# Optimization experiments

Hardware: AMD Instinct MI355X
Metric: run time of the kernel (lower is better)

The kernel has to match this reference:

```python
import jax, jax.numpy as jnp
import numpy as np

C = 1024
H = 16

def setup_inputs() -> dict:
    key = jax.random.key(0)
    ks = jax.random.split(key, 12)
    s = lambda d: 1.0 / np.sqrt(d)
    return {
        "x": jax.random.normal(ks[0], (2, 2048, C), dtype=jnp.float32),
        "ln1_g": jnp.ones((C,), jnp.float32),
        "ln1_b": jnp.zeros((C,), jnp.float32),
        "attn_w": jax.random.normal(ks[1], (C, 3 * C), jnp.float32) * s(C),
        "attn_b": jnp.zeros((3 * C,), jnp.float32),
        "proj_w": jax.random.normal(ks[2], (C, C), jnp.float32) * s(C),
        "proj_b": jnp.zeros((C,), jnp.float32),
        "ln2_g": jnp.ones((C,), jnp.float32),
        "ln2_b": jnp.zeros((C,), jnp.float32),
        "fc_w": jax.random.normal(ks[3], (C, 4 * C), jnp.float32) * s(C),
        "fc_b": jnp.zeros((4 * C,), jnp.float32),
        "fc2_w": jax.random.normal(ks[4], (4 * C, C), jnp.float32) * s(4 * C),
        "fc2_b": jnp.zeros((C,), jnp.float32),
    }

def _layernorm(x, g, b, eps=1e-5):
    mu = jnp.mean(x, axis=-1, keepdims=True)
    var = jnp.var(x, axis=-1, keepdims=True)
    return (x - mu) * jax.lax.rsqrt(var + eps) * g + b

def _attn(x, attn_w, attn_b, proj_w, proj_b):
    B, T, Cd = x.shape
    hd = Cd // H
    qkv = x @ attn_w + attn_b                      # [B,T,3C]
    q, k, v = jnp.split(qkv, 3, axis=-1)
    q = q.reshape(B, T, H, hd).transpose(0, 2, 1, 3)  # [B,H,T,hd]
    k = k.reshape(B, T, H, hd).transpose(0, 2, 1, 3)
    v = v.reshape(B, T, H, hd).transpose(0, 2, 1, 3)
    att = jnp.einsum("bhqd,bhkd->bhqk", q, k) * (1.0 / np.sqrt(hd))
    mask = jnp.tril(jnp.ones((T, T), bool))
    att = jnp.where(mask, att, -jnp.inf)
    att = jax.nn.softmax(att, axis=-1)
    y = jnp.einsum("bhqk,bhkd->bhqd", att, v)
    y = y.transpose(0, 2, 1, 3).reshape(B, T, Cd)
    return y @ proj_w + proj_b

def _mlp(x, fc_w, fc_b, fc2_w, fc2_b):
    h = jax.nn.gelu(x @ fc_w + fc_b, approximate=False)
    return h @ fc2_w + fc2_b

def reference(x, ln1_g, ln1_b, attn_w, attn_b, proj_w, proj_b,
              ln2_g, ln2_b, fc_w, fc_b, fc2_w, fc2_b):
    x = x + _attn(_layernorm(x, ln1_g, ln1_b), attn_w, attn_b, proj_w, proj_b)
    x = x + _mlp(_layernorm(x, ln2_g, ln2_b), fc_w, fc_b, fc2_w, fc2_b)
    return x
```

## Files before the change

### kernel.cpp

```cpp
#include <hip/hip_runtime.h>
#include <hip/hip_bf16.h>
#include <math.h>

typedef __attribute__((ext_vector_type(8))) short short8;
typedef __attribute__((ext_vector_type(4))) float f32x4;

#define C_DIM 1024
#define T_DIM 2048
#define NH 16
#define HD 64
#define NTOK 4096

__device__ __forceinline__ unsigned short f2bf(float f) {
  unsigned u = __float_as_uint(f);
  u += 0x7fffu + ((u >> 16) & 1u);
  return (unsigned short)(u >> 16);
}

__global__ __launch_bounds__(256) void ln_kernel(
    const float* __restrict__ x, const float* __restrict__ g,
    const float* __restrict__ b, unsigned short* __restrict__ out) {
  int row = blockIdx.x;
  int tid = threadIdx.x;
  const float4* xr = (const float4*)(x + (size_t)row * C_DIM);
  float4 v = xr[tid];
  float s = v.x + v.y + v.z + v.w;
  float ss = v.x * v.x + v.y * v.y + v.z * v.z + v.w * v.w;
#pragma unroll
  for (int off = 32; off; off >>= 1) {
    s += __shfl_down(s, off);
    ss += __shfl_down(ss, off);
  }
  __shared__ float red[8];
  if ((tid & 63) == 0) { red[tid >> 6] = s; red[4 + (tid >> 6)] = ss; }
  __syncthreads();
  float S = red[0] + red[1] + red[2] + red[3];
  float SS = red[4] + red[5] + red[6] + red[7];
  float mu = S * (1.0f / C_DIM);
  float var = SS * (1.0f / C_DIM) - mu * mu;
  float rs = rsqrtf(var + 1e-5f);
  float4 gg = ((const float4*)g)[tid];
  float4 bb = ((const float4*)b)[tid];
  ushort4 o;
  o.x = f2bf((v.x - mu) * rs * gg.x + bb.x);
  o.y = f2bf((v.y - mu) * rs * gg.y + bb.y);
  o.z = f2bf((v.z - mu) * rs * gg.z + bb.z);
  o.w = f2bf((v.w - mu) * rs * gg.w + bb.w);
  *(ushort4*)(out + (size_t)row * C_DIM + tid * 4) = o;
}

__global__ __launch_bounds__(256) void wt_kernel(
    const float* __restrict__ W, unsigned short* __restrict__ Wt, int K, int N) {
  __shared__ float t[32][33];
  int n0 = blockIdx.x * 32, k0 = blockIdx.y * 32;
  int tx = threadIdx.x, ty = threadIdx.y;
#pragma unroll
  for (int j = 0; j < 4; j++)
    t[ty + j * 8][tx] = W[(size_t)(k0 + ty + j * 8) * N + n0 + tx];
  __syncthreads();
#pragma unroll
  for (int j = 0; j < 4; j++)
    Wt[(size_t)(n0 + ty + j * 8) * K + k0 + tx] = f2bf(t[tx][ty + j * 8]);
}

template <int ACT, int OUTBF>
__global__ __launch_bounds__(256) void gemm_bt(
    const unsigned short* __restrict__ A, const unsigned short* __restrict__ Bt,
    const float* __restrict__ bias, const float* __restrict__ res,
    void* __restrict__ Cout, int M, int N, int K) {
  __shared__ short sA[128 * 32];
  __shared__ short sB[128 * 32];
  int tid = threadIdx.x;
  int wave = tid >> 6, lane = tid & 63;
  int l16 = lane & 15, quad = lane >> 4;
  int row0 = blockIdx.y * 128, col0 = blockIdx.x * 128;
  int wm = (wave & 1) * 64, wn = (wave >> 1) * 64;
  f32x4 acc[4][4];
#pragma unroll
  for (int i = 0; i < 4; i++)
#pragma unroll
    for (int j = 0; j < 4; j++) acc[i][j] = (f32x4){0.f, 0.f, 0.f, 0.f};

  for (int k0 = 0; k0 < K; k0 += 32) {
#pragma unroll
    for (int i = 0; i < 2; i++) {
      int c = tid + i * 256;
      int r = c >> 2, cc = (c & 3) * 8;
      *(uint4*)&sA[r * 32 + cc] = *(const uint4*)(A + (size_t)(row0 + r) * K + k0 + cc);
      *(uint4*)&sB[r * 32 + cc] = *(const uint4*)(Bt + (size_t)(col0 + r) * K + k0 + cc);
    }
    __syncthreads();
    short8 a[4], b[4];
#pragma unroll
    for (int i = 0; i < 4; i++) {
      a[i] = *(const short8*)&sA[(wm + i * 16 + l16) * 32 + quad * 8];
      b[i] = *(const short8*)&sB[(wn + i * 16 + l16) * 32 + quad * 8];
    }
#pragma unroll
    for (int mi = 0; mi < 4; mi++)
#pragma unroll
      for (int ni = 0; ni < 4; ni++)
        acc[mi][ni] = __builtin_amdgcn_mfma_f32_16x16x32_bf16(a[mi], b[ni], acc[mi][ni], 0, 0, 0);
    __syncthreads();
  }
#pragma unroll
  for (int mi = 0; mi < 4; mi++) {
#pragma unroll
    for (int ni = 0; ni < 4; ni++) {
      int col = col0 + wn + ni * 16 + l16;
      float bv = bias[col];
#pragma unroll
      for (int i = 0; i < 4; i++) {
        int row = row0 + wm + mi * 16 + quad * 4 + i;
        float v = acc[mi][ni][i] + bv;
        if (ACT == 1) v = 0.5f * v * (1.0f + erff(v * 0.7071067811865475f));
        if (res) v += res[(size_t)row * N + col];
        if (OUTBF)
          ((unsigned short*)Cout)[(size_t)row * N + col] = f2bf(v);
        else
          ((float*)Cout)[(size_t)row * N + col] = v;
      }
    }
  }
}

#define AP 72
__global__ __launch_bounds__(256) void attn_mfma_kernel(
    const unsigned short* __restrict__ qkv, unsigned short* __restrict__ Y) {
  __shared__ short sK[64 * AP];
  __shared__ short sVt[64 * AP];
  __shared__ short sP[4][16 * AP];
  int qt = gridDim.x - 1 - blockIdx.x;
  int hb = blockIdx.y;
  int bb = hb >> 4, h = hb & 15;
  int tid = threadIdx.x, wave = tid >> 6, lane = tid & 63;
  int l16 = lane & 15, quad = lane >> 4;
  int q0 = qt * 64, qbase = q0 + wave * 16;

  const unsigned short* qrow = qkv + (size_t)(bb * T_DIM + qbase + l16) * 3072 + h * HD;
  short8 qf[2];
  qf[0] = *(const short8*)(qrow + quad * 8);
  qf[1] = *(const short8*)(qrow + 32 + quad * 8);

  f32x4 o[4];
#pragma unroll
  for (int i = 0; i < 4; i++) o[i] = (f32x4){0.f, 0.f, 0.f, 0.f};
  float m = -1e30f, l = 0.f;

  const unsigned short* Kbase = qkv + (size_t)bb * T_DIM * 3072 + C_DIM + h * HD;
  const unsigned short* Vbase = Kbase + C_DIM;

  for (int kt = 0; kt <= qt; kt++) {
    int kv0 = kt * 64;
#pragma unroll
    for (int i = 0; i < 2; i++) {
      int c = tid + i * 256;
      int r = c >> 3, dcg = c & 7, dc = dcg * 8;
      uint4 kx = *(const uint4*)(Kbase + (size_t)(kv0 + r) * 3072 + dc);
      uint4 vx = *(const uint4*)(Vbase + (size_t)(kv0 + r) * 3072 + dc);
      *(uint4*)&sK[r * AP + dc] = kx;
      unsigned short ve[8];
      *(uint4*)ve = vx;
#pragma unroll
      for (int j = 0; j < 8; j++) {
        int jj = (j + r + dcg) & 7;
        sVt[(dc + jj) * AP + r] = (short)ve[jj];
      }
    }
    __syncthreads();

    f32x4 st[4];
#pragma unroll
    for (int i = 0; i < 4; i++) st[i] = (f32x4){0.f, 0.f, 0.f, 0.f};
#pragma unroll
    for (int kc = 0; kc < 2; kc++)
#pragma unroll
      for (int mt = 0; mt < 4; mt++) {
        short8 af = *(const short8*)&sK[(mt * 16 + l16) * AP + kc * 32 + quad * 8];
        st[mt] = __builtin_amdgcn_mfma_f32_16x16x32_bf16(af, qf[kc], st[mt], 0, 0, 0);
      }

    int qg = qbase + l16;
    float vals[16];
#pragma unroll
    for (int mt = 0; mt < 4; mt++)
#pragma unroll
      for (int r = 0; r < 4; r++) {
        int kv = kv0 + mt * 16 + quad * 4 + r;
        vals[mt * 4 + r] = (kv <= qg) ? st[mt][r] * 0.125f : -1e30f;
      }
    float mx = vals[0];
#pragma unroll
    for (int i = 1; i < 16; i++) mx = fmaxf(mx, vals[i]);
    mx = fmaxf(mx, __shfl_xor(mx, 16));
    mx = fmaxf(mx, __shfl_xor(mx, 32));
    float mnew = fmaxf(m, mx);
    float alpha = __expf(m - mnew);
    float ps = 0.f;
#pragma unroll
    for (int i = 0; i < 16; i++) {
      vals[i] = __expf(vals[i] - mnew);
      ps += vals[i];
    }
    ps += __shfl_xor(ps, 16);
    ps += __shfl_xor(ps, 32);
    l = l * alpha + ps;
    m = mnew;
#pragma unroll
    for (int r = 0; r < 4; r++) {
      float ar = __shfl(alpha, quad * 20 + r);
#pragma unroll
      for (int dt = 0; dt < 4; dt++) o[dt][r] *= ar;
    }

#pragma unroll
    for (int mt = 0; mt < 4; mt++) {
      ushort4 pw;
      pw.x = f2bf(vals[mt * 4 + 0]);
      pw.y = f2bf(vals[mt * 4 + 1]);
      pw.z = f2bf(vals[mt * 4 + 2]);
      pw.w = f2bf(vals[mt * 4 + 3]);
      *(ushort4*)&sP[wave][l16 * AP + mt * 16 + quad * 4] = pw;
    }

#pragma unroll
    for (int kc = 0; kc < 2; kc++) {
      short8 pa = *(const short8*)&sP[wave][l16 * AP + kc * 32 + quad * 8];
#pragma unroll
      for (int dt = 0; dt < 4; dt++) {
        short8 vb = *(const short8*)&sVt[(dt * 16 + l16) * AP + kc * 32 + quad * 8];
        o[dt] = __builtin_amdgcn_mfma_f32_16x16x32_bf16(pa, vb, o[dt], 0, 0, 0);
      }
    }
    __syncthreads();
  }

  float il[4];
#pragma unroll
  for (int r = 0; r < 4; r++) il[r] = 1.0f / __shfl(l, quad * 20 + r);
  unsigned short* Yb = Y + (size_t)(bb * T_DIM + qbase) * C_DIM + h * HD;
#pragma unroll
  for (int dt = 0; dt < 4; dt++)
#pragma unroll
    for (int r = 0; r < 4; r++)
      Yb[(size_t)(quad * 4 + r) * C_DIM + dt * 16 + l16] = f2bf(o[dt][r] * il[r]);
}

extern "C" void kernel_launch(void* const* d_in, const int* in_sizes, int n_in,
                              void* d_out, int out_size, void* d_ws, size_t ws_size,
                              hipStream_t stream) {
  const float* x      = (const float*)d_in[0];
  const float* ln1_g  = (const float*)d_in[1];
  const float* ln1_b  = (const float*)d_in[2];
  const float* attn_w = (const float*)d_in[3];
  const float* attn_b = (const float*)d_in[4];
  const float* proj_w = (const float*)d_in[5];
  const float* proj_b = (const float*)d_in[6];
  const float* ln2_g  = (const float*)d_in[7];
  const float* ln2_b  = (const float*)d_in[8];
  const float* fc_w   = (const float*)d_in[9];
  const float* fc_b   = (const float*)d_in[10];
  const float* fc2_w  = (const float*)d_in[11];
  const float* fc2_b  = (const float*)d_in[12];

  char* ws = (char*)d_ws;
  unsigned short* wqkv_t  = (unsigned short*)(ws + 0);
  unsigned short* wproj_t = (unsigned short*)(ws + 6291456);
  unsigned short* wfc_t   = (unsigned short*)(ws + 8388608);
  unsigned short* wfc2_t  = (unsigned short*)(ws + 16777216);
  unsigned short* xn1     = (unsigned short*)(ws + 25165824);
  unsigned short* qkv     = (unsigned short*)(ws + 33554432);
  unsigned short* y       = (unsigned short*)(ws + 58720256);
  unsigned short* hmid    = (unsigned short*)(ws + 33554432);
  unsigned short* xn2     = xn1;
  float* x1  = (float*)d_out;
  float* out = (float*)d_out;

  dim3 t32x8(32, 8);
  wt_kernel<<<dim3(3072 / 32, 1024 / 32), t32x8, 0, stream>>>(attn_w, wqkv_t, 1024, 3072);
  wt_kernel<<<dim3(1024 / 32, 1024 / 32), t32x8, 0, stream>>>(proj_w, wproj_t, 1024, 1024);
  wt_kernel<<<dim3(4096 / 32, 1024 / 32), t32x8, 0, stream>>>(fc_w, wfc_t, 1024, 4096);
  wt_kernel<<<dim3(1024 / 32, 4096 / 32), t32x8, 0, stream>>>(fc2_w, wfc2_t, 4096, 1024);

  ln_kernel<<<NTOK, 256, 0, stream>>>(x, ln1_g, ln1_b, xn1);
  gemm_bt<0, 1><<<dim3(3072 / 128, NTOK / 128), 256, 0, stream>>>(
      xn1, wqkv_t, attn_b, nullptr, qkv, NTOK, 3072, 1024);
  attn_mfma_kernel<<<dim3(T_DIM / 64, 32), 256, 0, stream>>>(qkv, y);
  gemm_bt<0, 0><<<dim3(1024 / 128, NTOK / 128), 256, 0, stream>>>(
      y, wproj_t, proj_b, x, (void*)x1, NTOK, 1024, 1024);
  ln_kernel<<<NTOK, 256, 0, stream>>>(x1, ln2_g, ln2_b, xn2);
  gemm_bt<1, 1><<<dim3(4096 / 128, NTOK / 128), 256, 0, stream>>>(
      xn2, wfc_t, fc_b, nullptr, hmid, NTOK, 4096, 1024);
  gemm_bt<0, 0><<<dim3(1024 / 128, NTOK / 128), 256, 0, stream>>>(
      hmid, wfc2_t, fc2_b, x1, (void*)out, NTOK, 1024, 4096);
}
```

Baseline: 493.2 us.

## Use direct global-to-LDS async loads in GEMM and attention K tiles

Result: slower. 526.2 us (+6.7%).

```diff
diff --git a/kernel.cpp b/kernel.cpp
--- a/kernel.cpp
+++ b/kernel.cpp
@@ -15,6 +15,12 @@
   unsigned u = __float_as_uint(f);
   u += 0x7fffu + ((u >> 16) & 1u);
   return (unsigned short)(u >> 16);
+}
+
+typedef __attribute__((address_space(1))) const unsigned int guint;
+typedef __attribute__((address_space(3))) unsigned int luint;
+__device__ __forceinline__ void async16(const void* g, void* l) {
+  __builtin_amdgcn_global_load_lds((guint*)g, (luint*)l, 16, 0, 0);
 }
 
 __global__ __launch_bounds__(256) void ln_kernel(
@@ -86,8 +92,8 @@
     for (int i = 0; i < 2; i++) {
       int c = tid + i * 256;
       int r = c >> 2, cc = (c & 3) * 8;
-      *(uint4*)&sA[r * 32 + cc] = *(const uint4*)(A + (size_t)(row0 + r) * K + k0 + cc);
-      *(uint4*)&sB[r * 32 + cc] = *(const uint4*)(Bt + (size_t)(col0 + r) * K + k0 + cc);
+      async16(A + (size_t)(row0 + r) * K + k0 + cc, &sA[c * 8]);
+      async16(Bt + (size_t)(col0 + r) * K + k0 + cc, &sB[c * 8]);
     }
     __syncthreads();
     short8 a[4], b[4];
@@ -127,7 +133,7 @@
 #define AP 72
 __global__ __launch_bounds__(256) void attn_mfma_kernel(
     const unsigned short* __restrict__ qkv, unsigned short* __restrict__ Y) {
-  __shared__ short sK[64 * AP];
+  __shared__ short sK[2 * 64 * 32];
   __shared__ short sVt[64 * AP];
   __shared__ short sP[4][16 * AP];
   int qt = gridDim.x - 1 - blockIdx.x;
@@ -135,7 +141,7 @@
   int bb = hb >> 4, h = hb & 15;
   int tid = threadIdx.x, wave = tid >> 6, lane = tid & 63;
   int l16 = lane & 15, quad = lane >> 4;
-  int q0 = qt * 64, qbase = q0 + wave * 16;
+  int qbase = qt * 64 + wave * 16;
 
   const unsigned short* qrow = qkv + (size_t)(bb * T_DIM + qbase + l16) * 3072 + h * HD;
   short8 qf[2];
@@ -155,10 +161,14 @@
 #pragma unroll
     for (int i = 0; i < 2; i++) {
       int c = tid + i * 256;
+      int kc = c >> 8, rem = c & 255, rr = rem >> 2, j = rem & 3;
+      async16(Kbase + (size_t)(kv0 + rr) * 3072 + kc * 32 + j * 8, &sK[c * 8]);
+    }
+#pragma unroll
+    for (int i = 0; i < 2; i++) {
+      int c = tid + i * 256;
       int r = c >> 3, dcg = c & 7, dc = dcg * 8;
-      uint4 kx = *(const uint4*)(Kbase + (size_t)(kv0 + r) * 3072 + dc);
       uint4 vx = *(const uint4*)(Vbase + (size_t)(kv0 + r) * 3072 + dc);
-      *(uint4*)&sK[r * AP + dc] = kx;
       unsigned short ve[8];
       *(uint4*)ve = vx;
 #pragma unroll
@@ -176,19 +186,26 @@
     for (int kc = 0; kc < 2; kc++)
 #pragma unroll
       for (int mt = 0; mt < 4; mt++) {
-        short8 af = *(const short8*)&sK[(mt * 16 + l16) * AP + kc * 32 + quad * 8];
+        short8 af = *(const short8*)&sK[kc * 2048 + (mt * 16 + l16) * 32 + quad * 8];
         st[mt] = __builtin_amdgcn_mfma_f32_16x16x32_bf16(af, qf[kc], st[mt], 0, 0, 0);
       }
 
-    int qg = qbase + l16;
     float vals[16];
-#pragma unroll
-    for (int mt = 0; mt < 4; mt++)
-#pragma unroll
-      for (int r = 0; r < 4; r++) {
-        int kv = kv0 + mt * 16 + quad * 4 + r;
-        vals[mt * 4 + r] = (kv <= qg) ? st[mt][r] * 0.125f : -1e30f;
-      }
+    if (kt == qt) {
+      int qg = qbase + l16;
+#pragma unroll
+      for (int mt = 0; mt < 4; mt++)
+#pragma unroll
+        for (int r = 0; r < 4; r++) {
+          int kv = kv0 + mt * 16 + quad * 4 + r;
+          vals[mt * 4 + r] = (kv <= qg) ? st[mt][r] * 0.125f : -1e30f;
+        }
+    } else {
+#pragma unroll
+      for (int mt = 0; mt < 4; mt++)
+#pragma unroll
+        for (int r = 0; r < 4; r++) vals[mt * 4 + r] = st[mt][r] * 0.125f;
+    }
     float mx = vals[0];
 #pragma unroll
     for (int i = 1; i < 16; i++) mx = fmaxf(mx, vals[i]);
```

## Register-prefetch next tiles in GEMM and attention, skip mask on full tiles

Applied to the files above, without the earlier changes.

Result: faster. 472.3 us (-4.2%).

```diff
diff --git a/kernel.cpp b/kernel.cpp
--- a/kernel.cpp
+++ b/kernel.cpp
@@ -81,15 +81,28 @@
 #pragma unroll
     for (int j = 0; j < 4; j++) acc[i][j] = (f32x4){0.f, 0.f, 0.f, 0.f};
 
+  int r1 = tid >> 2, cc1 = (tid & 3) * 8;
+  const unsigned short* Ap = A + (size_t)(row0 + r1) * K + cc1;
+  const unsigned short* Bp = Bt + (size_t)(col0 + r1) * K + cc1;
+  const size_t RSK = (size_t)64 * K;
+  uint4 pa0 = *(const uint4*)Ap;
+  uint4 pa1 = *(const uint4*)(Ap + RSK);
+  uint4 pb0 = *(const uint4*)Bp;
+  uint4 pb1 = *(const uint4*)(Bp + RSK);
+
   for (int k0 = 0; k0 < K; k0 += 32) {
-#pragma unroll
-    for (int i = 0; i < 2; i++) {
-      int c = tid + i * 256;
-      int r = c >> 2, cc = (c & 3) * 8;
-      *(uint4*)&sA[r * 32 + cc] = *(const uint4*)(A + (size_t)(row0 + r) * K + k0 + cc);
-      *(uint4*)&sB[r * 32 + cc] = *(const uint4*)(Bt + (size_t)(col0 + r) * K + k0 + cc);
-    }
+    if (k0) __syncthreads();
+    *(uint4*)&sA[r1 * 32 + cc1] = pa0;
+    *(uint4*)&sA[(r1 + 64) * 32 + cc1] = pa1;
+    *(uint4*)&sB[r1 * 32 + cc1] = pb0;
+    *(uint4*)&sB[(r1 + 64) * 32 + cc1] = pb1;
     __syncthreads();
+    if (k0 + 32 < K) {
+      pa0 = *(const uint4*)(Ap + k0 + 32);
+      pa1 = *(const uint4*)(Ap + RSK + k0 + 32);
+      pb0 = *(const uint4*)(Bp + k0 + 32);
+      pb1 = *(const uint4*)(Bp + RSK + k0 + 32);
+    }
     short8 a[4], b[4];
 #pragma unroll
     for (int i = 0; i < 4; i++) {
@@ -101,7 +114,6 @@
 #pragma unroll
       for (int ni = 0; ni < 4; ni++)
         acc[mi][ni] = __builtin_amdgcn_mfma_f32_16x16x32_bf16(a[mi], b[ni], acc[mi][ni], 0, 0, 0);
-    __syncthreads();
   }
 #pragma unroll
   for (int mi = 0; mi < 4; mi++) {
@@ -135,7 +147,7 @@
   int bb = hb >> 4, h = hb & 15;
   int tid = threadIdx.x, wave = tid >> 6, lane = tid & 63;
   int l16 = lane & 15, quad = lane >> 4;
-  int q0 = qt * 64, qbase = q0 + wave * 16;
+  int qbase = qt * 64 + wave * 16;
 
   const unsigned short* qrow = qkv + (size_t)(bb * T_DIM + qbase + l16) * 3072 + h * HD;
   short8 qf[2];
@@ -150,24 +162,46 @@
   const unsigned short* Kbase = qkv + (size_t)bb * T_DIM * 3072 + C_DIM + h * HD;
   const unsigned short* Vbase = Kbase + C_DIM;
 
+  int rr = tid >> 3, dcg = tid & 7, dc = dcg * 8;
+  const unsigned short* Kp = Kbase + (size_t)rr * 3072 + dc;
+  const unsigned short* Vp = Vbase + (size_t)rr * 3072 + dc;
+  const size_t HROW = (size_t)32 * 3072;
+  const size_t TS = (size_t)64 * 3072;
+
+  uint4 kx0 = *(const uint4*)Kp;
+  uint4 kx1 = *(const uint4*)(Kp + HROW);
+  uint4 vx0 = *(const uint4*)Vp;
+  uint4 vx1 = *(const uint4*)(Vp + HROW);
+
   for (int kt = 0; kt <= qt; kt++) {
     int kv0 = kt * 64;
-#pragma unroll
-    for (int i = 0; i < 2; i++) {
-      int c = tid + i * 256;
-      int r = c >> 3, dcg = c & 7, dc = dcg * 8;
-      uint4 kx = *(const uint4*)(Kbase + (size_t)(kv0 + r) * 3072 + dc);
-      uint4 vx = *(const uint4*)(Vbase + (size_t)(kv0 + r) * 3072 + dc);
-      *(uint4*)&sK[r * AP + dc] = kx;
+    if (kt) __syncthreads();
+    *(uint4*)&sK[rr * AP + dc] = kx0;
+    *(uint4*)&sK[(rr + 32) * AP + dc] = kx1;
+    {
       unsigned short ve[8];
-      *(uint4*)ve = vx;
+      *(uint4*)ve = vx0;
 #pragma unroll
       for (int j = 0; j < 8; j++) {
-        int jj = (j + r + dcg) & 7;
-        sVt[(dc + jj) * AP + r] = (short)ve[jj];
+        int jj = (j + rr + dcg) & 7;
+        sVt[(dc + jj) * AP + rr] = (short)ve[jj];
+      }
+      *(uint4*)ve = vx1;
+#pragma unroll
+      for (int j = 0; j < 8; j++) {
+        int jj = (j + rr + 32 + dcg) & 7;
+        sVt[(dc + jj) * AP + rr + 32] = (short)ve[jj];
       }
     }
     __syncthreads();
+    if (kt < qt) {
+      const unsigned short* Kn = Kp + (size_t)(kt + 1) * TS;
+      const unsigned short* Vn = Vp + (size_t)(kt + 1) * TS;
+      kx0 = *(const uint4*)Kn;
+      kx1 = *(const uint4*)(Kn + HROW);
+      vx0 = *(const uint4*)Vn;
+      vx1 = *(const uint4*)(Vn + HROW);
+    }
 
     f32x4 st[4];
 #pragma unroll
@@ -180,15 +214,22 @@
         st[mt] = __builtin_amdgcn_mfma_f32_16x16x32_bf16(af, qf[kc], st[mt], 0, 0, 0);
       }
 
-    int qg = qbase + l16;
     float vals[16];
-#pragma unroll
-    for (int mt = 0; mt < 4; mt++)
-#pragma unroll
-      for (int r = 0; r < 4; r++) {
-        int kv = kv0 + mt * 16 + quad * 4 + r;
-        vals[mt * 4 + r] = (kv <= qg) ? st[mt][r] * 0.125f : -1e30f;
-      }
+    if (kt == qt) {
+      int qg = qbase + l16;
+#pragma unroll
+      for (int mt = 0; mt < 4; mt++)
+#pragma unroll
+        for (int r = 0; r < 4; r++) {
+          int kv = kv0 + mt * 16 + quad * 4 + r;
+          vals[mt * 4 + r] = (kv <= qg) ? st[mt][r] * 0.125f : -1e30f;
+        }
+    } else {
+#pragma unroll
+      for (int mt = 0; mt < 4; mt++)
+#pragma unroll
+        for (int r = 0; r < 4; r++) vals[mt * 4 + r] = st[mt][r] * 0.125f;
+    }
     float mx = vals[0];
 #pragma unroll
     for (int i = 1; i < 16; i++) mx = fmaxf(mx, vals[i]);
@@ -232,7 +273,6 @@
         o[dt] = __builtin_amdgcn_mfma_f32_16x16x32_bf16(pa, vb, o[dt], 0, 0, 0);
       }
     }
-    __syncthreads();
   }
 
   float il[4];
```

## Prefetch GEMM tiles into registers, pair attention query tiles, add narrow-N GEMM

Applied to the files above, without the earlier changes.

Result: faster. 399.8 us (-18.9%).

```diff
diff --git a/kernel.cpp b/kernel.cpp
--- a/kernel.cpp
+++ b/kernel.cpp
@@ -81,15 +81,28 @@
 #pragma unroll
     for (int j = 0; j < 4; j++) acc[i][j] = (f32x4){0.f, 0.f, 0.f, 0.f};
 
+  int r1 = tid >> 2, cc1 = (tid & 3) * 8;
+  const unsigned short* Ap = A + (size_t)(row0 + r1) * K + cc1;
+  const unsigned short* Bp = Bt + (size_t)(col0 + r1) * K + cc1;
+  const size_t RSK = (size_t)64 * K;
+  uint4 pa0 = *(const uint4*)Ap;
+  uint4 pa1 = *(const uint4*)(Ap + RSK);
+  uint4 pb0 = *(const uint4*)Bp;
+  uint4 pb1 = *(const uint4*)(Bp + RSK);
+
   for (int k0 = 0; k0 < K; k0 += 32) {
-#pragma unroll
-    for (int i = 0; i < 2; i++) {
-      int c = tid + i * 256;
-      int r = c >> 2, cc = (c & 3) * 8;
-      *(uint4*)&sA[r * 32 + cc] = *(const uint4*)(A + (size_t)(row0 + r) * K + k0 + cc);
-      *(uint4*)&sB[r * 32 + cc] = *(const uint4*)(Bt + (size_t)(col0 + r) * K + k0 + cc);
-    }
+    if (k0) __syncthreads();
+    *(uint4*)&sA[r1 * 32 + cc1] = pa0;
+    *(uint4*)&sA[(r1 + 64) * 32 + cc1] = pa1;
+    *(uint4*)&sB[r1 * 32 + cc1] = pb0;
+    *(uint4*)&sB[(r1 + 64) * 32 + cc1] = pb1;
     __syncthreads();
+    if (k0 + 32 < K) {
+      pa0 = *(const uint4*)(Ap + k0 + 32);
+      pa1 = *(const uint4*)(Ap + RSK + k0 + 32);
+      pb0 = *(const uint4*)(Bp + k0 + 32);
+      pb1 = *(const uint4*)(Bp + RSK + k0 + 32);
+    }
     short8 a[4], b[4];
 #pragma unroll
     for (int i = 0; i < 4; i++) {
@@ -101,7 +114,6 @@
 #pragma unroll
       for (int ni = 0; ni < 4; ni++)
         acc[mi][ni] = __builtin_amdgcn_mfma_f32_16x16x32_bf16(a[mi], b[ni], acc[mi][ni], 0, 0, 0);
-    __syncthreads();
   }
 #pragma unroll
   for (int mi = 0; mi < 4; mi++) {
@@ -124,34 +136,190 @@
   }
 }
 
+template <int ACT, int OUTBF>
+__global__ __launch_bounds__(256) void gemm_bt64(
+    const unsigned short* __restrict__ A, const unsigned short* __restrict__ Bt,
+    const float* __restrict__ bias, const float* __restrict__ res,
+    void* __restrict__ Cout, int M, int N, int K) {
+  __shared__ short sA[128 * 32];
+  __shared__ short sB[64 * 32];
+  int tid = threadIdx.x;
+  int wave = tid >> 6, lane = tid & 63;
+  int l16 = lane & 15, quad = lane >> 4;
+  int row0 = blockIdx.y * 128, col0 = blockIdx.x * 64;
+  int wm = (wave & 1) * 64, wn = (wave >> 1) * 32;
+  f32x4 acc[4][2];
+#pragma unroll
+  for (int i = 0; i < 4; i++)
+#pragma unroll
+    for (int j = 0; j < 2; j++) acc[i][j] = (f32x4){0.f, 0.f, 0.f, 0.f};
+
+  int r1 = tid >> 2, cc1 = (tid & 3) * 8;
+  const unsigned short* Ap = A + (size_t)(row0 + r1) * K + cc1;
+  const unsigned short* Bp = Bt + (size_t)(col0 + r1) * K + cc1;
+  const size_t RSK = (size_t)64 * K;
+  uint4 pa0 = *(const uint4*)Ap;
+  uint4 pa1 = *(const uint4*)(Ap + RSK);
+  uint4 pb0 = *(const uint4*)Bp;
+
+  for (int k0 = 0; k0 < K; k0 += 32) {
+    if (k0) __syncthreads();
+    *(uint4*)&sA[r1 * 32 + cc1] = pa0;
+    *(uint4*)&sA[(r1 + 64) * 32 + cc1] = pa1;
+    *(uint4*)&sB[r1 * 32 + cc1] = pb0;
+    __syncthreads();
+    if (k0 + 32 < K) {
+      pa0 = *(const uint4*)(Ap + k0 + 32);
+      pa1 = *(const uint4*)(Ap + RSK + k0 + 32);
+      pb0 = *(const uint4*)(Bp + k0 + 32);
+    }
+    short8 a[4], b[2];
+#pragma unroll
+    for (int i = 0; i < 4; i++)
+      a[i] = *(const short8*)&sA[(wm + i * 16 + l16) * 32 + quad * 8];
+#pragma unroll
+    for (int i = 0; i < 2; i++)
+      b[i] = *(const short8*)&sB[(wn + i * 16 + l16) * 32 + quad * 8];
+#pragma unroll
+    for (int mi = 0; mi < 4; mi++)
+#pragma unroll
+      for (int ni = 0; ni < 2; ni++)
+        acc[mi][ni] = __builtin_amdgcn_mfma_f32_16x16x32_bf16(a[mi], b[ni], acc[mi][ni], 0, 0, 0);
+  }
+#pragma unroll
+  for (int mi = 0; mi < 4; mi++) {
+#pragma unroll
+    for (int ni = 0; ni < 2; ni++) {
+      int col = col0 + wn + ni * 16 + l16;
+      float bv = bias[col];
+#pragma unroll
+      for (int i = 0; i < 4; i++) {
+        int row = row0 + wm + mi * 16 + quad * 4 + i;
+        float v = acc[mi][ni][i] + bv;
+        if (ACT == 1) v = 0.5f * v * (1.0f + erff(v * 0.7071067811865475f));
+        if (res) v += res[(size_t)row * N + col];
+        if (OUTBF)
+          ((unsigned short*)Cout)[(size_t)row * N + col] = f2bf(v);
+        else
+          ((float*)Cout)[(size_t)row * N + col] = v;
+      }
+    }
+  }
+}
+
 #define AP 72
+struct AttnState {
+  f32x4 o[4];
+  float m, l;
+};
+
+__device__ __forceinline__ void attn_tile_compute(
+    const short* __restrict__ sK, const short* __restrict__ sVt,
+    short* __restrict__ sPw, const short8* qf, int qg, int kv0, int diag,
+    AttnState& S, int l16, int quad) {
+  f32x4 st[4];
+#pragma unroll
+  for (int i = 0; i < 4; i++) st[i] = (f32x4){0.f, 0.f, 0.f, 0.f};
+#pragma unroll
+  for (int kc = 0; kc < 2; kc++)
+#pragma unroll
+    for (int mt = 0; mt < 4; mt++) {
+      short8 af = *(const short8*)&sK[(mt * 16 + l16) * AP + kc * 32 + quad * 8];
+      st[mt] = __builtin_amdgcn_mfma_f32_16x16x32_bf16(af, qf[kc], st[mt], 0, 0, 0);
+    }
+  float vals[16];
+  if (diag) {
+#pragma unroll
+    for (int mt = 0; mt < 4; mt++)
+#pragma unroll
+      for (int r = 0; r < 4; r++) {
+        int kv = kv0 + mt * 16 + quad * 4 + r;
+        vals[mt * 4 + r] = (kv <= qg) ? st[mt][r] * 0.125f : -1e30f;
+      }
+  } else {
+#pragma unroll
+    for (int mt = 0; mt < 4; mt++)
+#pragma unroll
+      for (int r = 0; r < 4; r++) vals[mt * 4 + r] = st[mt][r] * 0.125f;
+  }
+  float mx = vals[0];
+#pragma unroll
+  for (int i = 1; i < 16; i++) mx = fmaxf(mx, vals[i]);
+  mx = fmaxf(mx, __shfl_xor(mx, 16));
+  mx = fmaxf(mx, __shfl_xor(mx, 32));
+  float mnew = fmaxf(S.m, mx);
+  float alpha = __expf(S.m - mnew);
+  float ps = 0.f;
+#pragma unroll
+  for (int i = 0; i < 16; i++) {
+    vals[i] = __expf(vals[i] - mnew);
+    ps += vals[i];
+  }
+  ps += __shfl_xor(ps, 16);
+  ps += __shfl_xor(ps, 32);
+  S.l = S.l * alpha + ps;
+  S.m = mnew;
+#pragma unroll
+  for (int r = 0; r < 4; r++) {
+    float ar = __shfl(alpha, quad * 20 + r);
+#pragma unroll
+    for (int dt = 0; dt < 4; dt++) S.o[dt][r] *= ar;
+  }
+#pragma unroll
+  for (int mt = 0; mt < 4; mt++) {
+    ushort4 pw;
+    pw.x = f2bf(vals[mt * 4 + 0]);
+    pw.y = f2bf(vals[mt * 4 + 1]);
+    pw.z = f2bf(vals[mt * 4 + 2]);
+    pw.w = f2bf(vals[mt * 4 + 3]);
+    *(ushort4*)&sPw[l16 * AP + mt * 16 + quad * 4] = pw;
+  }
+#pragma unroll
+  for (int kc = 0; kc < 2; kc++) {
+    short8 pa = *(const short8*)&sPw[l16 * AP + kc * 32 + quad * 8];
+#pragma unroll
+    for (int dt = 0; dt < 4; dt++) {
+      short8 vb = *(const short8*)&sVt[(dt * 16 + l16) * AP + kc * 32 + quad * 8];
+      S.o[dt] = __builtin_amdgcn_mfma_f32_16x16x32_bf16(pa, vb, S.o[dt], 0, 0, 0);
+    }
+  }
+}
+
 __global__ __launch_bounds__(256) void attn_mfma_kernel(
     const unsigned short* __restrict__ qkv, unsigned short* __restrict__ Y) {
   __shared__ short sK[64 * AP];
   __shared__ short sVt[64 * AP];
   __shared__ short sP[4][16 * AP];
-  int qt = gridDim.x - 1 - blockIdx.x;
+  int p = blockIdx.x;
   int hb = blockIdx.y;
   int bb = hb >> 4, h = hb & 15;
   int tid = threadIdx.x, wave = tid >> 6, lane = tid & 63;
   int l16 = lane & 15, quad = lane >> 4;
-  int q0 = qt * 64, qbase = q0 + wave * 16;
-
-  const unsigned short* qrow = qkv + (size_t)(bb * T_DIM + qbase + l16) * 3072 + h * HD;
-  short8 qf[2];
-  qf[0] = *(const short8*)(qrow + quad * 8);
-  qf[1] = *(const short8*)(qrow + 32 + quad * 8);
-
-  f32x4 o[4];
-#pragma unroll
-  for (int i = 0; i < 4; i++) o[i] = (f32x4){0.f, 0.f, 0.f, 0.f};
-  float m = -1e30f, l = 0.f;
+  int qtA = p, qtB = 31 - p;
+  int qbA = qtA * 64 + wave * 16, qbB = qtB * 64 + wave * 16;
+
+  const unsigned short* qrowA = qkv + (size_t)(bb * T_DIM + qbA + l16) * 3072 + h * HD;
+  const unsigned short* qrowB = qkv + (size_t)(bb * T_DIM + qbB + l16) * 3072 + h * HD;
+  short8 qfA[2], qfB[2];
+  qfA[0] = *(const short8*)(qrowA + quad * 8);
+  qfA[1] = *(const short8*)(qrowA + 32 + quad * 8);
+  qfB[0] = *(const short8*)(qrowB + quad * 8);
+  qfB[1] = *(const short8*)(qrowB + 32 + quad * 8);
+
+  AttnState SA, SB;
+#pragma unroll
+  for (int i = 0; i < 4; i++) {
+    SA.o[i] = (f32x4){0.f, 0.f, 0.f, 0.f};
+    SB.o[i] = (f32x4){0.f, 0.f, 0.f, 0.f};
+  }
+  SA.m = -1e30f; SA.l = 0.f; SB.m = -1e30f; SB.l = 0.f;
 
   const unsigned short* Kbase = qkv + (size_t)bb * T_DIM * 3072 + C_DIM + h * HD;
   const unsigned short* Vbase = Kbase + C_DIM;
 
-  for (int kt = 0; kt <= qt; kt++) {
+  for (int kt = 0; kt <= qtB; kt++) {
     int kv0 = kt * 64;
+    if (kt) __syncthreads();
 #pragma unroll
     for (int i = 0; i < 2; i++) {
       int c = tid + i * 256;
@@ -169,81 +337,26 @@
     }
     __syncthreads();
 
-    f32x4 st[4];
-#pragma unroll
-    for (int i = 0; i < 4; i++) st[i] = (f32x4){0.f, 0.f, 0.f, 0.f};
-#pragma unroll
-    for (int kc = 0; kc < 2; kc++)
-#pragma unroll
-      for (int mt = 0; mt < 4; mt++) {
-        short8 af = *(const short8*)&sK[(mt * 16 + l16) * AP + kc * 32 + quad * 8];
-        st[mt] = __builtin_amdgcn_mfma_f32_16x16x32_bf16(af, qf[kc], st[mt], 0, 0, 0);
-      }
-
-    int qg = qbase + l16;
-    float vals[16];
-#pragma unroll
-    for (int mt = 0; mt < 4; mt++)
-#pragma unroll
-      for (int r = 0; r < 4; r++) {
-        int kv = kv0 + mt * 16 + quad * 4 + r;
-        vals[mt * 4 + r] = (kv <= qg) ? st[mt][r] * 0.125f : -1e30f;
-      }
-    float mx = vals[0];
-#pragma unroll
-    for (int i = 1; i < 16; i++) mx = fmaxf(mx, vals[i]);
-    mx = fmaxf(mx, __shfl_xor(mx, 16));
-    mx = fmaxf(mx, __shfl_xor(mx, 32));
-    float mnew = fmaxf(m, mx);
-    float alpha = __expf(m - mnew);
-    float ps = 0.f;
-#pragma unroll
-    for (int i = 0; i < 16; i++) {
-      vals[i] = __expf(vals[i] - mnew);
-      ps += vals[i];
-    }
-    ps += __shfl_xor(ps, 16);
-    ps += __shfl_xor(ps, 32);
-    l = l * alpha + ps;
-    m = mnew;
+    attn_tile_compute(sK, sVt, sP[wave], qfB, qbB + l16, kv0, kt == qtB, SB, l16, quad);
+    if (kt <= qtA)
+      attn_tile_compute(sK, sVt, sP[wave], qfA, qbA + l16, kv0, kt == qtA, SA, l16, quad);
+  }
+
+  float ilA[4], ilB[4];
+#pragma unroll
+  for (int r = 0; r < 4; r++) {
+    ilA[r] = 1.0f / __shfl(SA.l, quad * 20 + r);
+    ilB[r] = 1.0f / __shfl(SB.l, quad * 20 + r);
+  }
+  unsigned short* YA = Y + (size_t)(bb * T_DIM + qbA) * C_DIM + h * HD;
+  unsigned short* YB = Y + (size_t)(bb * T_DIM + qbB) * C_DIM + h * HD;
+#pragma unroll
+  for (int dt = 0; dt < 4; dt++)
 #pragma unroll
     for (int r = 0; r < 4; r++) {
-      float ar = __shfl(alpha, quad * 20 + r);
-#pragma unroll
-      for (int dt = 0; dt < 4; dt++) o[dt][r] *= ar;
-    }
-
-#pragma unroll
-    for (int mt = 0; mt < 4; mt++) {
-      ushort4 pw;
-      pw.x = f2bf(vals[mt * 4 + 0]);
-      pw.y = f2bf(vals[mt * 4 + 1]);
-      pw.z = f2bf(vals[mt * 4 + 2]);
-      pw.w = f2bf(vals[mt * 4 + 3]);
-      *(ushort4*)&sP[wave][l16 * AP + mt * 16 + quad * 4] = pw;
-    }
-
-#pragma unroll
-    for (int kc = 0; kc < 2; kc++) {
-      short8 pa = *(const short8*)&sP[wave][l16 * AP + kc * 32 + quad * 8];
-#pragma unroll
-      for (int dt = 0; dt < 4; dt++) {
-        short8 vb = *(const short8*)&sVt[(dt * 16 + l16) * AP + kc * 32 + quad * 8];
-        o[dt] = __builtin_amdgcn_mfma_f32_16x16x32_bf16(pa, vb, o[dt], 0, 0, 0);
-      }
-    }
-    __syncthreads();
-  }
-
-  float il[4];
-#pragma unroll
-  for (int r = 0; r < 4; r++) il[r] = 1.0f / __shfl(l, quad * 20 + r);
-  unsigned short* Yb = Y + (size_t)(bb * T_DIM + qbase) * C_DIM + h * HD;
-#pragma unroll
-  for (int dt = 0; dt < 4; dt++)
-#pragma unroll
-    for (int r = 0; r < 4; r++)
-      Yb[(size_t)(quad * 4 + r) * C_DIM + dt * 16 + l16] = f2bf(o[dt][r] * il[r]);
+      YA[(size_t)(quad * 4 + r) * C_DIM + dt * 16 + l16] = f2bf(SA.o[dt][r] * ilA[r]);
+      YB[(size_t)(quad * 4 + r) * C_DIM + dt * 16 + l16] = f2bf(SB.o[dt][r] * ilB[r]);
+    }
 }
 
 extern "C" void kernel_launch(void* const* d_in, const int* in_sizes, int n_in,
@@ -285,12 +398,12 @@
   ln_kernel<<<NTOK, 256, 0, stream>>>(x, ln1_g, ln1_b, xn1);
   gemm_bt<0, 1><<<dim3(3072 / 128, NTOK / 128), 256, 0, stream>>>(
       xn1, wqkv_t, attn_b, nullptr, qkv, NTOK, 3072, 1024);
-  attn_mfma_kernel<<<dim3(T_DIM / 64, 32), 256, 0, stream>>>(qkv, y);
-  gemm_bt<0, 0><<<dim3(1024 / 128, NTOK / 128), 256, 0, stream>>>(
+  attn_mfma_kernel<<<dim3(16, 32), 256, 0, stream>>>(qkv, y);
+  gemm_bt64<0, 0><<<dim3(1024 / 64, NTOK / 128), 256, 0, stream>>>(
       y, wproj_t, proj_b, x, (void*)x1, NTOK, 1024, 1024);
   ln_kernel<<<NTOK, 256, 0, stream>>>(x1, ln2_g, ln2_b, xn2);
   gemm_bt<1, 1><<<dim3(4096 / 128, NTOK / 128), 256, 0, stream>>>(
       xn2, wfc_t, fc_b, nullptr, hmid, NTOK, 4096, 1024);
-  gemm_bt<0, 0><<<dim3(1024 / 128, NTOK / 128), 256, 0, stream>>>(
+  gemm_bt64<0, 0><<<dim3(1024 / 64, NTOK / 128), 256, 0, stream>>>(
       hmid, wfc2_t, fc2_b, x1, (void*)out, NTOK, 1024, 4096);
 }
```
